# Kernel tuning notes

Hardware: AMD Instinct MI355X
Metric: run time of the kernel (lower is better)

The kernel has to match this reference:

```python
import jax, jax.numpy as jnp
import numpy as np

K = 4  # top-k from init
BN_IS_FOLDED = True  # BatchNorm (eval mode) folded into per-channel scale s and shift t


def tconv(x, W):
    # x: (b, C, v, n); W: (Cout, Cin, 3) temporal conv, kernel (3,1,1), padding (1,0,0), no bias
    return jax.lax.conv_general_dilated(
        x, W[:, :, :, None], window_strides=(1, 1),
        padding=((1, 1), (0, 0)), dimension_numbers=('NCHW', 'OIHW', 'NCHW'))


def gcn_single(xn, src, dst, Wg, bg):
    # PyG GCNConv: add self-loops, symmetric normalization, then scatter-add.
    N = xn.shape[0]
    xl = xn @ Wg  # (N, C)
    loop = jnp.arange(N, dtype=src.dtype)
    s = jnp.concatenate([src, loop])
    d = jnp.concatenate([dst, loop])
    deg = jax.ops.segment_sum(jnp.ones(s.shape[0], dtype=xn.dtype), d, num_segments=N)
    dinv = jnp.where(deg > 0, jax.lax.rsqrt(deg), 0.0)
    norm = dinv[s] * dinv[d]
    out = jax.ops.segment_sum(norm[:, None] * xl[s], d, num_segments=N)
    return out + bg


def setup_inputs() -> dict:
    key = jax.random.key(0)
    ks = jax.random.split(key, 10)
    C = 256
    x = jax.random.normal(ks[0], (512, C, 16, 16), dtype=jnp.float32)
    Wd = jax.random.normal(ks[1], (C, C, 3), dtype=jnp.float32) * 0.02
    s1 = 1.0 + 0.1 * jax.random.normal(ks[2], (C,), dtype=jnp.float32)
    t1 = 0.1 * jax.random.normal(ks[3], (C,), dtype=jnp.float32)
    Wg = jax.random.normal(ks[4], (C, C), dtype=jnp.float32) * 0.02
    bg = 0.01 * jax.random.normal(ks[5], (C,), dtype=jnp.float32)
    Wu = jax.random.normal(ks[6], (C, C, 3), dtype=jnp.float32) * 0.02
    s2 = 1.0 + 0.1 * jax.random.normal(ks[7], (C,), dtype=jnp.float32)
    t2 = 0.1 * jax.random.normal(ks[8], (C,), dtype=jnp.float32)
    return {"x": x, "batch": 4, "Wd": Wd, "s1": s1, "t1": t1,
            "Wg": Wg, "bg": bg, "Wu": Wu, "s2": s2, "t2": t2}


def reference(x, batch, Wd, s1, t1, Wg, bg, Wu, s2, t2):
    tlen, c, h, w = x.shape
    b = batch
    v = tlen // b
    hw = h * w
    # (tlen,c,h,w) -> (b,c,v,h*w)
    x4 = x.reshape(b, v, c, h, w).transpose(0, 2, 1, 3, 4).reshape(b, c, v, hw)
    xd = tconv(x4, Wd) * s1[None, :, None, None] + t1[None, :, None, None]  # down_conv + BN(eval)

    # --- dynamic graph build (no-grad in original) ---
    f = jax.lax.stop_gradient(xd).transpose(0, 2, 3, 1)  # (b, v, hw, c)
    f1, f2 = f[:, :-1], f[:, 1:]                          # (b, t_1, hw, c)
    t_1 = v - 1
    sq1 = jnp.sum(f1 * f1, axis=-1)                       # (b,t_1,hw)
    sq2 = jnp.sum(f2 * f2, axis=-1)
    dots = jnp.einsum('btnc,btmc->btnm', f1, f2)
    d2 = jnp.maximum(sq1[..., :, None] + sq2[..., None, :] - 2.0 * dots, 0.0)
    sim = -jnp.sqrt(d2).reshape(b, t_1, hw * hw)
    sim = sim / jnp.maximum(jnp.linalg.norm(sim, axis=-1, keepdims=True), 1e-12)  # F.normalize
    sim = jnp.where(sim < 0.05, 100.0, sim)
    _, idx = jax.lax.top_k(sim, K)                        # (b, t_1, K)
    frame = jnp.arange(t_1, dtype=jnp.int32)[None, :, None]
    row = (idx // hw).astype(jnp.int32) + frame * hw
    col = (idx % hw).astype(jnp.int32) + (frame + 1) * hw
    row = row.reshape(b, -1)
    col = col.reshape(b, -1)
    src = jnp.concatenate([row, col], axis=1)             # forward + reversed edges
    dst = jnp.concatenate([col, row], axis=1)

    # --- per-sample GCN (batched with vmap) ---
    nodes = xd.transpose(0, 2, 3, 1).reshape(b, v * hw, c)  # 'b c v n -> b (v n) c'
    out = jax.vmap(lambda xn, s, d: gcn_single(xn, s, d, Wg, bg))(nodes, src, dst)

    # --- up path ---
    o4 = out.transpose(0, 2, 1).reshape(b, c, v, hw)
    xu = tconv(o4, Wu) * s2[None, :, None, None] + t2[None, :, None, None]
    return xu.reshape(b, c, v, h, w).transpose(0, 2, 1, 3, 4).reshape(tlen, c, h, w)
```

## Files before the change

kernel.cpp:

```cpp
#include <hip/hip_runtime.h>

typedef __attribute__((ext_vector_type(8))) short short8;
typedef __attribute__((ext_vector_type(4))) float f32x4;
typedef unsigned short u16;
typedef unsigned int u32;

__device__ __forceinline__ void gld_lds16(const void* g, void* l) {
  __builtin_amdgcn_global_load_lds((const __attribute__((address_space(1))) void*)g,
                                   (__attribute__((address_space(3))) void*)l,
                                   16, 0, 0);
}

__device__ __forceinline__ u16 f2b(float x) {
  union { float f; u32 u; } v; v.f = x;
  u32 u = v.u;
  return (u16)((u + 0x7FFFu + ((u >> 16) & 1u)) >> 16);
}
__device__ __forceinline__ float b2f(u16 x) {
  union { u32 u; float f; } v; v.u = ((u32)x) << 16; return v.f;
}
__device__ __forceinline__ u32 pack_pair(float lo, float hi) {
  return (u32)f2b(lo) | ((u32)f2b(hi) << 16);
}

__global__ __launch_bounds__(256) void k_pack(const float* __restrict__ Wd, const float* __restrict__ Wg,
                                              const float* __restrict__ Wu,
                                              u16* __restrict__ Wdp, u16* __restrict__ WgT,
                                              u16* __restrict__ Wup) {
  int id = blockIdx.x * 256 + threadIdx.x;
  if (id < 196608) {
    int kk = id >> 16;
    int rem = id & 65535;
    int co = rem >> 8, ci = rem & 255;
    u32 s = (u32)co * 768 + (u32)ci * 3 + kk;
    Wdp[id] = f2b(Wd[s]);
    Wup[id] = f2b(Wu[s]);
  } else {
    int id2 = id - 196608;
    int j = id2 >> 8, i = id2 & 255;
    WgT[id2] = f2b(Wg[i * 256 + j]);
  }
}

__global__ __launch_bounds__(256) void k_transpose(const float* __restrict__ x, u16* __restrict__ xT) {
  __shared__ u16 tile[64][72];
  int blk = blockIdx.x;
  int tl = blk >> 4;
  int sub = blk & 15;
  int ci0 = (sub >> 2) << 6;
  int p0 = (sub & 3) << 6;
  int tid = threadIdx.x;
  int i = tid >> 2;
  int ch = tid & 3;
  const float* gsrc = x + (size_t)tl * 65536 + (ci0 + i) * 256 + p0 + ch * 16;
  __align__(16) u16 cv[16];
#pragma unroll
  for (int v4 = 0; v4 < 4; ++v4) {
    float4 f = *(const float4*)(gsrc + v4 * 4);
    cv[v4 * 4 + 0] = f2b(f.x);
    cv[v4 * 4 + 1] = f2b(f.y);
    cv[v4 * 4 + 2] = f2b(f.z);
    cv[v4 * 4 + 3] = f2b(f.w);
  }
  *(uint4*)&tile[i][ch * 16] = *(const uint4*)&cv[0];
  *(uint4*)&tile[i][ch * 16 + 8] = *(const uint4*)&cv[8];
  __syncthreads();
  __align__(16) u16 tmp[16];
#pragma unroll
  for (int cc = 0; cc < 16; ++cc) tmp[cc] = tile[ch * 16 + cc][i];
  u16* gdst = xT + (size_t)tl * 65536 + (p0 + i) * 256 + ci0 + ch * 16;
  *(uint4*)(gdst) = *(const uint4*)&tmp[0];
  *(uint4*)(gdst + 8) = *(const uint4*)&tmp[8];
}

__device__ __forceinline__ void stage_tile(const u16* __restrict__ g, int ldg, u16* s, int w, int lane) {
  int r = lane >> 2;
  int cc = (lane & 3) * 8;
#pragma unroll
  for (int j = 0; j < 2; ++j) {
    gld_lds16(g + (w * 32 + j * 16 + r) * ldg + cc, s + (w * 32 + j * 16) * 32);
  }
}

__device__ __forceinline__ void mfma_tiles(const u16* sA, const u16* sB, f32x4 acc[4][4],
                                           int wr, int wc, int lane) {
  int m16 = lane & 15;
  int q8 = (lane >> 4) * 8;
  short8 a[4], b[4];
#pragma unroll
  for (int mi = 0; mi < 4; ++mi) a[mi] = *(const short8*)(sA + (wr * 64 + mi * 16 + m16) * 32 + q8);
#pragma unroll
  for (int ni = 0; ni < 4; ++ni) b[ni] = *(const short8*)(sB + (wc * 64 + ni * 16 + m16) * 32 + q8);
#pragma unroll
  for (int mi = 0; mi < 4; ++mi)
#pragma unroll
    for (int ni = 0; ni < 4; ++ni)
      acc[mi][ni] = __builtin_amdgcn_mfma_f32_16x16x32_bf16(a[mi], b[ni], acc[mi][ni], 0, 0, 0);
}

__device__ __forceinline__ void store_pairs(u16* base, int row0, int stride, int colb,
                                            const float v[4], bool ev) {
  float pv[4];
#pragma unroll
  for (int r = 0; r < 4; ++r) pv[r] = __shfl_xor(v[r], 1, 64);
  u32 wd0 = ev ? pack_pair(v[0], pv[0]) : pack_pair(pv[0], v[0]);
  u32 wd1 = ev ? pack_pair(v[1], pv[1]) : pack_pair(pv[1], v[1]);
  u32 wd2 = ev ? pack_pair(v[2], pv[2]) : pack_pair(pv[2], v[2]);
  u32 wd3 = ev ? pack_pair(v[3], pv[3]) : pack_pair(pv[3], v[3]);
  u32 wa = ev ? wd0 : wd2;
  u32 wb = ev ? wd1 : wd3;
  int rs = ev ? 0 : 2;
  *(u32*)(base + (size_t)(row0 + rs) * stride + colb) = wa;
  *(u32*)(base + (size_t)(row0 + rs + 1) * stride + colb) = wb;
}

__device__ __forceinline__ void store_pairs_f32(float* base, int row0, int stride, int colb,
                                                const float v[4], bool ev) {
  float pv[4];
#pragma unroll
  for (int r = 0; r < 4; ++r) pv[r] = __shfl_xor(v[r], 1, 64);
  float2 wa, wb;
  if (ev) { wa = make_float2(v[0], pv[0]); wb = make_float2(v[1], pv[1]); }
  else    { wa = make_float2(pv[2], v[2]); wb = make_float2(pv[3], v[3]); }
  int rs = ev ? 0 : 2;
  *(float2*)(base + (size_t)(row0 + rs) * stride + colb) = wa;
  *(float2*)(base + (size_t)(row0 + rs + 1) * stride + colb) = wb;
}

__global__ __launch_bounds__(256) void k_g1(const u16* __restrict__ xT, const u16* __restrict__ Wdp,
                                            const float* __restrict__ s1, const float* __restrict__ t1,
                                            u16* __restrict__ nodes) {
  __shared__ u16 sA[128 * 32];
  __shared__ u16 sB[128 * 32];
  int blk = blockIdx.x;
  int bt = blk >> 2;
  int tile = blk & 3;
  int tm = tile >> 1, tn = tile & 1;
  int t = bt & 127;
  int tid = threadIdx.x, lane = tid & 63, w = tid >> 6;
  int wr = w >> 1, wc = w & 1;
  f32x4 acc[4][4];
#pragma unroll
  for (int i = 0; i < 4; ++i)
#pragma unroll
    for (int j = 0; j < 4; ++j) acc[i][j] = (f32x4){0.f, 0.f, 0.f, 0.f};

#pragma unroll
  for (int kk = 0; kk < 3; ++kk) {
    int tp = t - 1 + kk;
    if (tp < 0 || tp > 127) continue;
    const u16* gA = xT + ((size_t)(bt - t + tp) * 256 + tm * 128) * 256;
    const u16* gB = Wdp + (size_t)kk * 65536 + (tn * 128) * 256;
    for (int ks = 0; ks < 8; ++ks) {
      stage_tile(gA + ks * 32, 256, sA, w, lane);
      stage_tile(gB + ks * 32, 256, sB, w, lane);
      __syncthreads();
      mfma_tiles(sA, sB, acc, wr, wc, lane);
      __syncthreads();
    }
  }
  int q = lane >> 4, c = lane & 15;
  bool ev = (lane & 1) == 0;
  float s1v[4], t1v[4];
#pragma unroll
  for (int ni = 0; ni < 4; ++ni) {
    int co = tn * 128 + wc * 64 + ni * 16 + c;
    s1v[ni] = s1[co];
    t1v[ni] = t1[co];
  }
  u16* obase = nodes + (size_t)bt * 65536;
#pragma unroll
  for (int mi = 0; mi < 4; ++mi) {
    int row0 = tm * 128 + wr * 64 + mi * 16 + q * 4;
#pragma unroll
    for (int ni = 0; ni < 4; ++ni) {
      float v[4];
#pragma unroll
      for (int r = 0; r < 4; ++r) v[r] = acc[mi][ni][r] * s1v[ni] + t1v[ni];
      int colb = tn * 128 + wc * 64 + ni * 16 + (c & ~1);
      store_pairs(obase, row0, 256, colb, v, ev);
    }
  }
}

__global__ __launch_bounds__(256) void k_g2(const u16* __restrict__ nodes, const u16* __restrict__ WgT,
                                            const float* __restrict__ bg,
                                            u16* __restrict__ outp, float* __restrict__ edge) {
  __shared__ u16 sA[128 * 32];
  __shared__ u16 sB[128 * 32];
  int blk = blockIdx.x;
  int mt = blk >> 1;
  int nt = blk & 1;
  int m0 = mt * 128;
  int tid = threadIdx.x, lane = tid & 63, w = tid >> 6;
  int wr = w >> 1, wc = w & 1;
  f32x4 acc[4][4];
#pragma unroll
  for (int i = 0; i < 4; ++i)
#pragma unroll
    for (int j = 0; j < 4; ++j) acc[i][j] = (f32x4){0.f, 0.f, 0.f, 0.f};

  const u16* gA = nodes + (size_t)m0 * 256;
  const u16* gB = WgT + (size_t)(nt * 128) * 256;
  for (int ks = 0; ks < 8; ++ks) {
    stage_tile(gA + ks * 32, 256, sA, w, lane);
    stage_tile(gB + ks * 32, 256, sB, w, lane);
    __syncthreads();
    mfma_tiles(sA, sB, acc, wr, wc, lane);
    __syncthreads();
  }
  int q = lane >> 4, c = lane & 15;
  bool ev = (lane & 1) == 0;
  float bgv[4];
#pragma unroll
  for (int ni = 0; ni < 4; ++ni) bgv[ni] = bg[nt * 128 + wc * 64 + ni * 16 + c];
  int bt = m0 >> 8;
  bool eblk = ((m0 & 255) == 0) && (wr == 0) && (q == 0);
  u16* obase = outp + (size_t)m0 * 256;
#pragma unroll
  for (int mi = 0; mi < 4; ++mi) {
    int row0 = wr * 64 + mi * 16 + q * 4;
#pragma unroll
    for (int ni = 0; ni < 4; ++ni) {
      float raw[4], v[4];
#pragma unroll
      for (int r = 0; r < 4; ++r) { raw[r] = acc[mi][ni][r]; v[r] = raw[r] + bgv[ni]; }
      int colb = nt * 128 + wc * 64 + ni * 16 + (c & ~1);
      store_pairs(obase, row0, 256, colb, v, ev);
      if (eblk && mi == 0) {
        store_pairs_f32(edge + (size_t)bt * 1024, 0, 256, colb, raw, ev);
      }
    }
  }
}

__device__ __forceinline__ float dinv0(int t) {
  if (t == 0) return 0.44721359549995793f;
  if (t == 127) return 0.7071067811865476f;
  return 0.4082482904638631f;
}
__global__ __launch_bounds__(256) void k_fix(const float* __restrict__ edge, const float* __restrict__ bg,
                                             u16* __restrict__ outp) {
  int bt = blockIdx.x;
  int t = bt & 127;
  int j = threadIdx.x;
  const float ISQ2 = 0.7071067811865476f;
  float bgv = bg[j];
  float e_t = edge[(size_t)bt * 1024 + j];
  float At = dinv0(t);
  float o0 = bgv + At * At * e_t;
  if (t <= 126) {
    float At1 = dinv0(t + 1);
    const float* en = edge + (size_t)(bt + 1) * 1024;
    float s = At1 * en[j] + ISQ2 * (en[256 + j] + en[512 + j] + en[768 + j]);
    o0 += At * s;
  }
  float em1 = 0.f, Atm1 = 0.f;
  if (t >= 1) {
    Atm1 = dinv0(t - 1);
    em1 = edge[(size_t)(bt - 1) * 1024 + j];
    o0 += At * Atm1 * em1;
  }
  u16* ob = outp + (size_t)bt * 65536;
  ob[j] = f2b(o0);
#pragma unroll
  for (int k = 1; k <= 3; ++k) {
    float m = edge[(size_t)bt * 1024 + k * 256 + j];
    float ok = (t == 0) ? (bgv + m) : (bgv + 0.5f * m + ISQ2 * Atm1 * em1);
    ob[k * 256 + j] = f2b(ok);
  }
}

__global__ __launch_bounds__(256) void k_g3(const u16* __restrict__ outp, const u16* __restrict__ Wup,
                                            const float* __restrict__ s2, const float* __restrict__ t2,
                                            float* __restrict__ y) {
  __shared__ u16 sA[128 * 32];
  __shared__ u16 sB[128 * 32];
  __shared__ float ss2[128], st2[128];
  int blk = blockIdx.x;
  int bt = blk >> 2;
  int tile = blk & 3;
  int tm = tile >> 1, tn = tile & 1;
  int t = bt & 127;
  int tid = threadIdx.x, lane = tid & 63, w = tid >> 6;
  int wr = w >> 1, wc = w & 1;
  if (tid < 128) {
    int co = tm * 128 + tid;
    ss2[tid] = s2[co];
    st2[tid] = t2[co];
  }
  f32x4 acc[4][4];
#pragma unroll
  for (int i = 0; i < 4; ++i)
#pragma unroll
    for (int j = 0; j < 4; ++j) acc[i][j] = (f32x4){0.f, 0.f, 0.f, 0.f};

#pragma unroll
  for (int kk = 0; kk < 3; ++kk) {
    int tp = t - 1 + kk;
    if (tp < 0 || tp > 127) continue;
    const u16* gA = Wup + (size_t)kk * 65536 + (tm * 128) * 256;
    const u16* gB = outp + ((size_t)(bt - t + tp) * 256 + tn * 128) * 256;
    for (int ks = 0; ks < 8; ++ks) {
      stage_tile(gA + ks * 32, 256, sA, w, lane);
      stage_tile(gB + ks * 32, 256, sB, w, lane);
      __syncthreads();
      mfma_tiles(sA, sB, acc, wr, wc, lane);
      __syncthreads();
    }
  }
  int q = lane >> 4, c = lane & 15;
  bool ev = (lane & 1) == 0;
  float* ybase = y + (size_t)bt * 65536;
#pragma unroll
  for (int mi = 0; mi < 4; ++mi) {
    int rl = wr * 64 + mi * 16 + q * 4;
    float sv[4], tv[4];
#pragma unroll
    for (int r = 0; r < 4; ++r) { sv[r] = ss2[rl + r]; tv[r] = st2[rl + r]; }
#pragma unroll
    for (int ni = 0; ni < 4; ++ni) {
      float v[4];
#pragma unroll
      for (int r = 0; r < 4; ++r) v[r] = acc[mi][ni][r] * sv[r] + tv[r];
      int colb = tn * 128 + wc * 64 + ni * 16 + (c & ~1);
      store_pairs_f32(ybase, tm * 128 + rl, 256, colb, v, ev);
    }
  }
}

extern "C" void kernel_launch(void* const* d_in, const int* in_sizes, int n_in,
                              void* d_out, int out_size, void* d_ws, size_t ws_size,
                              hipStream_t stream) {
  (void)in_sizes; (void)n_in; (void)out_size; (void)ws_size;
  const float* x  = (const float*)d_in[0];
  const float* Wd = (const float*)d_in[2];
  const float* s1 = (const float*)d_in[3];
  const float* t1 = (const float*)d_in[4];
  const float* Wg = (const float*)d_in[5];
  const float* bg = (const float*)d_in[6];
  const float* Wu = (const float*)d_in[7];
  const float* s2 = (const float*)d_in[8];
  const float* t2 = (const float*)d_in[9];
  float* y = (float*)d_out;
  char* ws = (char*)d_ws;
  u16*   xT    = (u16*)(ws);
  u16*   nodes = (u16*)(ws + 67108864);
  float* edge  = (float*)(ws + 134217728);
  u16*   Wdp   = (u16*)(ws + 136314880);
  u16*   Wup   = (u16*)(ws + 136708096);
  u16*   WgT   = (u16*)(ws + 137101312);
  u16*   outp  = xT;

  k_pack<<<dim3(1024), dim3(256), 0, stream>>>(Wd, Wg, Wu, Wdp, WgT, Wup);
  k_transpose<<<dim3(8192), dim3(256), 0, stream>>>(x, xT);
  k_g1<<<dim3(2048), dim3(256), 0, stream>>>(xT, Wdp, s1, t1, nodes);
  k_g2<<<dim3(2048), dim3(256), 0, stream>>>(nodes, WgT, bg, outp, edge);
  k_fix<<<dim3(512), dim3(256), 0, stream>>>(edge, bg, outp);
  k_g3<<<dim3(2048), dim3(256), 0, stream>>>(outp, Wup, s2, t2, y);
}
```

Baseline: 467.9 us.

## Fold GCN weight into down-conv weights to drop the node GEMM

Precomputes a combined per-tap weight, Wg^T·diag(s1)·Wd, with a small GEMM kernel, plus a bias term (t1·Wg + bg). The down temporal conv and the GCN linear layer then run as one GEMM, which removes the separate nodes GEMM and its bf16 intermediate round trip through memory. The fused and up GEMMs also stage 64-wide K slices per barrier instead of 32, halving the number of sync points. The trade-off is extra rounding from storing the combined weights in bf16, and larger LDS tiles that may lower occupancy.

```diff
diff --git a/kernel.cpp b/kernel.cpp
--- a/kernel.cpp
+++ b/kernel.cpp
@@ -23,22 +23,34 @@
   return (u32)f2b(lo) | ((u32)f2b(hi) << 16);
 }
 
-__global__ __launch_bounds__(256) void k_pack(const float* __restrict__ Wd, const float* __restrict__ Wg,
+__global__ __launch_bounds__(256) void k_prep(const float* __restrict__ Wd, const float* __restrict__ Wg,
                                               const float* __restrict__ Wu,
-                                              u16* __restrict__ Wdp, u16* __restrict__ WgT,
-                                              u16* __restrict__ Wup) {
-  int id = blockIdx.x * 256 + threadIdx.x;
+                                              const float* __restrict__ s1, const float* __restrict__ t1,
+                                              const float* __restrict__ bg,
+                                              u16* __restrict__ WdT, u16* __restrict__ Wup,
+                                              u16* __restrict__ WgS,
+                                              float* __restrict__ c0, float* __restrict__ tWg) {
+  int blk = blockIdx.x;
+  int tid = threadIdx.x;
+  if (blk == 1024) {
+    int j = tid;
+    float a = 0.f;
+    for (int co = 0; co < 256; ++co) a += t1[co] * Wg[co * 256 + j];
+    tWg[j] = a;
+    c0[j] = a + bg[j];
+    return;
+  }
+  int id = blk * 256 + tid;
   if (id < 196608) {
     int kk = id >> 16;
     int rem = id & 65535;
-    int co = rem >> 8, ci = rem & 255;
-    u32 s = (u32)co * 768 + (u32)ci * 3 + kk;
-    Wdp[id] = f2b(Wd[s]);
-    Wup[id] = f2b(Wu[s]);
+    int a = rem >> 8, b = rem & 255;
+    Wup[id] = f2b(Wu[(u32)a * 768 + (u32)b * 3 + kk]);
+    WdT[id] = f2b(Wd[(u32)b * 768 + (u32)a * 3 + kk]);
   } else {
     int id2 = id - 196608;
-    int j = id2 >> 8, i = id2 & 255;
-    WgT[id2] = f2b(Wg[i * 256 + j]);
+    int j = id2 >> 8, co = id2 & 255;
+    WgS[id2] = f2b(Wg[co * 256 + j] * s1[co]);
   }
 }
 
@@ -127,11 +139,52 @@
   *(float2*)(base + (size_t)(row0 + rs + 1) * stride + colb) = wb;
 }
 
-__global__ __launch_bounds__(256) void k_g1(const u16* __restrict__ xT, const u16* __restrict__ Wdp,
-                                            const float* __restrict__ s1, const float* __restrict__ t1,
-                                            u16* __restrict__ nodes) {
+__global__ __launch_bounds__(256) void k_wcomb(const u16* __restrict__ WgS, const u16* __restrict__ WdT,
+                                               u16* __restrict__ Wcomb) {
   __shared__ u16 sA[128 * 32];
   __shared__ u16 sB[128 * 32];
+  int blk = blockIdx.x;
+  int kk = blk >> 2;
+  int tile = blk & 3;
+  int tm = tile >> 1, tn = tile & 1;
+  int tid = threadIdx.x, lane = tid & 63, w = tid >> 6;
+  int wr = w >> 1, wc = w & 1;
+  f32x4 acc[4][4];
+#pragma unroll
+  for (int i = 0; i < 4; ++i)
+#pragma unroll
+    for (int j = 0; j < 4; ++j) acc[i][j] = (f32x4){0.f, 0.f, 0.f, 0.f};
+  const u16* gA = WgS + (size_t)(tm * 128) * 256;
+  const u16* gB = WdT + (size_t)kk * 65536 + (size_t)(tn * 128) * 256;
+  for (int ks = 0; ks < 8; ++ks) {
+    stage_tile(gA + ks * 32, 256, sA, w, lane);
+    stage_tile(gB + ks * 32, 256, sB, w, lane);
+    __syncthreads();
+    mfma_tiles(sA, sB, acc, wr, wc, lane);
+    __syncthreads();
+  }
+  int q = lane >> 4, c = lane & 15;
+  bool ev = (lane & 1) == 0;
+  u16* obase = Wcomb + (size_t)kk * 65536;
+#pragma unroll
+  for (int mi = 0; mi < 4; ++mi) {
+    int row0 = tm * 128 + wr * 64 + mi * 16 + q * 4;
+#pragma unroll
+    for (int ni = 0; ni < 4; ++ni) {
+      float v[4];
+#pragma unroll
+      for (int r = 0; r < 4; ++r) v[r] = acc[mi][ni][r];
+      int colb = tn * 128 + wc * 64 + ni * 16 + (c & ~1);
+      store_pairs(obase, row0, 256, colb, v, ev);
+    }
+  }
+}
+
+__global__ __launch_bounds__(256) void k_g12(const u16* __restrict__ xT, const u16* __restrict__ Wcomb,
+                                             const float* __restrict__ c0, const float* __restrict__ tWg,
+                                             u16* __restrict__ outp, float* __restrict__ edge) {
+  __shared__ u16 sA[128 * 64];
+  __shared__ u16 sB[128 * 64];
   int blk = blockIdx.x;
   int bt = blk >> 2;
   int tile = blk & 3;
@@ -150,25 +203,29 @@
     int tp = t - 1 + kk;
     if (tp < 0 || tp > 127) continue;
     const u16* gA = xT + ((size_t)(bt - t + tp) * 256 + tm * 128) * 256;
-    const u16* gB = Wdp + (size_t)kk * 65536 + (tn * 128) * 256;
-    for (int ks = 0; ks < 8; ++ks) {
-      stage_tile(gA + ks * 32, 256, sA, w, lane);
-      stage_tile(gB + ks * 32, 256, sB, w, lane);
+    const u16* gB = Wcomb + (size_t)kk * 65536 + (size_t)(tn * 128) * 256;
+    for (int ks = 0; ks < 4; ++ks) {
+      stage_tile(gA + ks * 64, 256, sA, w, lane);
+      stage_tile(gA + ks * 64 + 32, 256, sA + 4096, w, lane);
+      stage_tile(gB + ks * 64, 256, sB, w, lane);
+      stage_tile(gB + ks * 64 + 32, 256, sB + 4096, w, lane);
       __syncthreads();
       mfma_tiles(sA, sB, acc, wr, wc, lane);
+      mfma_tiles(sA + 4096, sB + 4096, acc, wr, wc, lane);
       __syncthreads();
     }
   }
   int q = lane >> 4, c = lane & 15;
   bool ev = (lane & 1) == 0;
-  float s1v[4], t1v[4];
+  float c0v[4], tWgv[4];
 #pragma unroll
   for (int ni = 0; ni < 4; ++ni) {
-    int co = tn * 128 + wc * 64 + ni * 16 + c;
-    s1v[ni] = s1[co];
-    t1v[ni] = t1[co];
-  }
-  u16* obase = nodes + (size_t)bt * 65536;
+    int j = tn * 128 + wc * 64 + ni * 16 + c;
+    c0v[ni] = c0[j];
+    tWgv[ni] = tWg[j];
+  }
+  bool eblk = (tm == 0) && (wr == 0) && (q == 0);
+  u16* obase = outp + (size_t)bt * 65536;
 #pragma unroll
   for (int mi = 0; mi < 4; ++mi) {
     int row0 = tm * 128 + wr * 64 + mi * 16 + q * 4;
@@ -176,59 +233,14 @@
     for (int ni = 0; ni < 4; ++ni) {
       float v[4];
 #pragma unroll
-      for (int r = 0; r < 4; ++r) v[r] = acc[mi][ni][r] * s1v[ni] + t1v[ni];
+      for (int r = 0; r < 4; ++r) v[r] = acc[mi][ni][r] + c0v[ni];
       int colb = tn * 128 + wc * 64 + ni * 16 + (c & ~1);
       store_pairs(obase, row0, 256, colb, v, ev);
-    }
-  }
-}
-
-__global__ __launch_bounds__(256) void k_g2(const u16* __restrict__ nodes, const u16* __restrict__ WgT,
-                                            const float* __restrict__ bg,
-                                            u16* __restrict__ outp, float* __restrict__ edge) {
-  __shared__ u16 sA[128 * 32];
-  __shared__ u16 sB[128 * 32];
-  int blk = blockIdx.x;
-  int mt = blk >> 1;
-  int nt = blk & 1;
-  int m0 = mt * 128;
-  int tid = threadIdx.x, lane = tid & 63, w = tid >> 6;
-  int wr = w >> 1, wc = w & 1;
-  f32x4 acc[4][4];
-#pragma unroll
-  for (int i = 0; i < 4; ++i)
-#pragma unroll
-    for (int j = 0; j < 4; ++j) acc[i][j] = (f32x4){0.f, 0.f, 0.f, 0.f};
-
-  const u16* gA = nodes + (size_t)m0 * 256;
-  const u16* gB = WgT + (size_t)(nt * 128) * 256;
-  for (int ks = 0; ks < 8; ++ks) {
-    stage_tile(gA + ks * 32, 256, sA, w, lane);
-    stage_tile(gB + ks * 32, 256, sB, w, lane);
-    __syncthreads();
-    mfma_tiles(sA, sB, acc, wr, wc, lane);
-    __syncthreads();
-  }
-  int q = lane >> 4, c = lane & 15;
-  bool ev = (lane & 1) == 0;
-  float bgv[4];
-#pragma unroll
-  for (int ni = 0; ni < 4; ++ni) bgv[ni] = bg[nt * 128 + wc * 64 + ni * 16 + c];
-  int bt = m0 >> 8;
-  bool eblk = ((m0 & 255) == 0) && (wr == 0) && (q == 0);
-  u16* obase = outp + (size_t)m0 * 256;
-#pragma unroll
-  for (int mi = 0; mi < 4; ++mi) {
-    int row0 = wr * 64 + mi * 16 + q * 4;
-#pragma unroll
-    for (int ni = 0; ni < 4; ++ni) {
-      float raw[4], v[4];
-#pragma unroll
-      for (int r = 0; r < 4; ++r) { raw[r] = acc[mi][ni][r]; v[r] = raw[r] + bgv[ni]; }
-      int colb = nt * 128 + wc * 64 + ni * 16 + (c & ~1);
-      store_pairs(obase, row0, 256, colb, v, ev);
       if (eblk && mi == 0) {
-        store_pairs_f32(edge + (size_t)bt * 1024, 0, 256, colb, raw, ev);
+        float vE[4];
+#pragma unroll
+        for (int r = 0; r < 4; ++r) vE[r] = acc[0][ni][r] + tWgv[ni];
+        store_pairs_f32(edge + (size_t)bt * 1024, 0, 256, colb, vE, ev);
       }
     }
   }
@@ -274,8 +286,8 @@
 __global__ __launch_bounds__(256) void k_g3(const u16* __restrict__ outp, const u16* __restrict__ Wup,
                                             const float* __restrict__ s2, const float* __restrict__ t2,
                                             float* __restrict__ y) {
-  __shared__ u16 sA[128 * 32];
-  __shared__ u16 sB[128 * 32];
+  __shared__ u16 sA[128 * 64];
+  __shared__ u16 sB[128 * 64];
   __shared__ float ss2[128], st2[128];
   int blk = blockIdx.x;
   int bt = blk >> 2;
@@ -299,13 +311,16 @@
   for (int kk = 0; kk < 3; ++kk) {
     int tp = t - 1 + kk;
     if (tp < 0 || tp > 127) continue;
-    const u16* gA = Wup + (size_t)kk * 65536 + (tm * 128) * 256;
+    const u16* gA = Wup + (size_t)kk * 65536 + (size_t)(tm * 128) * 256;
     const u16* gB = outp + ((size_t)(bt - t + tp) * 256 + tn * 128) * 256;
-    for (int ks = 0; ks < 8; ++ks) {
-      stage_tile(gA + ks * 32, 256, sA, w, lane);
-      stage_tile(gB + ks * 32, 256, sB, w, lane);
+    for (int ks = 0; ks < 4; ++ks) {
+      stage_tile(gA + ks * 64, 256, sA, w, lane);
+      stage_tile(gA + ks * 64 + 32, 256, sA + 4096, w, lane);
+      stage_tile(gB + ks * 64, 256, sB, w, lane);
+      stage_tile(gB + ks * 64 + 32, 256, sB + 4096, w, lane);
       __syncthreads();
       mfma_tiles(sA, sB, acc, wr, wc, lane);
+      mfma_tiles(sA + 4096, sB + 4096, acc, wr, wc, lane);
       __syncthreads();
     }
   }
@@ -344,18 +359,20 @@
   const float* t2 = (const float*)d_in[9];
   float* y = (float*)d_out;
   char* ws = (char*)d_ws;
-  u16*   xT    = (u16*)(ws);
-  u16*   nodes = (u16*)(ws + 67108864);
+  u16*   outp  = (u16*)(ws);
+  u16*   xT    = (u16*)(ws + 67108864);
   float* edge  = (float*)(ws + 134217728);
-  u16*   Wdp   = (u16*)(ws + 136314880);
-  u16*   Wup   = (u16*)(ws + 136708096);
-  u16*   WgT   = (u16*)(ws + 137101312);
-  u16*   outp  = xT;
-
-  k_pack<<<dim3(1024), dim3(256), 0, stream>>>(Wd, Wg, Wu, Wdp, WgT, Wup);
+  u16*   WdT   = (u16*)(ws + 134217728);
+  u16*   WgS   = (u16*)(ws + 134611072);
+  u16*   Wup   = (u16*)(ws + 136314880);
+  u16*   Wcomb = (u16*)(ws + 136708096);
+  float* c0    = (float*)(ws + 137101312);
+  float* tWg   = (float*)(ws + 137102336);
+
+  k_prep<<<dim3(1025), dim3(256), 0, stream>>>(Wd, Wg, Wu, s1, t1, bg, WdT, Wup, WgS, c0, tWg);
+  k_wcomb<<<dim3(12), dim3(256), 0, stream>>>(WgS, WdT, Wcomb);
   k_transpose<<<dim3(8192), dim3(256), 0, stream>>>(x, xT);
-  k_g1<<<dim3(2048), dim3(256), 0, stream>>>(xT, Wdp, s1, t1, nodes);
-  k_g2<<<dim3(2048), dim3(256), 0, stream>>>(nodes, WgT, bg, outp, edge);
+  k_g12<<<dim3(2048), dim3(256), 0, stream>>>(xT, Wcomb, c0, tWg, outp, edge);
   k_fix<<<dim3(512), dim3(256), 0, stream>>>(edge, bg, outp);
   k_g3<<<dim3(2048), dim3(256), 0, stream>>>(outp, Wup, s2, t2, y);
 }
```

Result: faster. 429.2 us (-8.3%).
